# Optimization experiments

Hardware: AMD Instinct MI355X
Metric: run time of the kernel (lower is better)

Reference implementation:

```python
import jax, jax.numpy as jnp
import numpy as np

D_MODEL = 768
NUM_HEADS = 12


def setup_inputs() -> dict:
    key = jax.random.key(0)
    ks = jax.random.split(key, 11)
    B, N, D = 4, 2048, D_MODEL
    s = 1.0 / np.sqrt(D)
    return {
        "q": jax.random.normal(ks[0], (B, N, D), jnp.float32),
        "k": jax.random.normal(ks[1], (B, N, D), jnp.float32),
        "v": jax.random.normal(ks[2], (B, N, D), jnp.float32),
        "wq": jax.random.normal(ks[3], (D, D), jnp.float32) * s,
        "bq": jnp.zeros((D,), jnp.float32),
        "wk": jax.random.normal(ks[4], (D, D), jnp.float32) * s,
        "bk": jnp.zeros((D,), jnp.float32),
        "wv": jax.random.normal(ks[5], (D, D), jnp.float32) * s,
        "bv": jnp.zeros((D,), jnp.float32),
        "wo": jax.random.normal(ks[6], (D, D), jnp.float32) * s,
        "bo": jnp.zeros((D,), jnp.float32),
    }


def _split_heads(x, num_heads):
    B, N, D = x.shape
    hd = D // num_heads
    return x.reshape(B, N, num_heads, hd).transpose(0, 2, 1, 3)  # (B,H,N,hd)


def reference(q, k, v, wq, bq, wk, bk, wv, bv, wo, bo):
    B, N, D = q.shape
    H = NUM_HEADS
    qw = q @ wq.T + bq
    kw = k @ wk.T + bk
    vw = v @ wv.T + bv
    hq = _split_heads(qw, H)
    hk = _split_heads(kw, H)
    hv = _split_heads(vw, H)
    scale = 1.0 / jnp.sqrt(jnp.asarray(hq.shape[-1], hq.dtype))
    scores = jnp.einsum("bhnd,bhmd->bhnm", hq, hk) * scale  # (B,H,N,N) explicit
    attn = jax.nn.softmax(scores, axis=-1)
    out = jnp.einsum("bhnm,bhmd->bhnd", attn, hv)
    out = out.transpose(0, 2, 1, 3).reshape(B, N, D)
    return out @ wo.T + bo
```

## Files before the change

### kernel.cpp

```cpp
#include <hip/hip_runtime.h>
#include <hip/hip_bf16.h>
#include <type_traits>


typedef __attribute__((ext_vector_type(8)))  __bf16 bf16x8;
typedef __attribute__((ext_vector_type(4)))  __bf16 bf16x4;
typedef __attribute__((ext_vector_type(4)))  float  f32x4;
typedef __attribute__((ext_vector_type(16))) float  f32x16;
typedef __attribute__((ext_vector_type(2)))  unsigned u32x2;
typedef __attribute__((ext_vector_type(4)))  unsigned u32x4;

#define NH  12
#define HD  64
#define DM  768
#define SEQ 2048
#define NB  4
#define M8  8192
#define ALPHA 0.18033688011112043f

__device__ __forceinline__ f32x4 mfma16(bf16x8 a, bf16x8 b, f32x4 c) {
  return __builtin_amdgcn_mfma_f32_16x16x32_bf16(a, b, c, 0, 0, 0);
}
__device__ __forceinline__ f32x16 mfma32(bf16x8 a, bf16x8 b, f32x16 c) {
  return __builtin_amdgcn_mfma_f32_32x32x16_bf16(a, b, c, 0, 0, 0);
}
__device__ __forceinline__ void gload16(const void* g, void* l) {
  auto gp = (__attribute__((address_space(1))) void*)(const_cast<void*>(g));
  auto lp = (__attribute__((address_space(3))) void*)(l);
  __builtin_amdgcn_global_load_lds(gp, lp, 16, 0, 0);
}
__device__ __forceinline__ float exp2_(float x) {
#if __has_builtin(__builtin_amdgcn_exp2f)
  return __builtin_amdgcn_exp2f(x);
#else
  return exp2f(x);
#endif
}

#define VMLG(n) do { asm volatile("s_waitcnt vmcnt(" #n ") lgkmcnt(0)" ::: "memory"); \
                     __builtin_amdgcn_sched_barrier(0); } while (0)
#define VMW(n) do { asm volatile("s_waitcnt vmcnt(" #n ")" ::: "memory"); \
                    __builtin_amdgcn_sched_barrier(0); } while (0)
#define BARX do { __builtin_amdgcn_s_barrier(); \
                  __builtin_amdgcn_sched_barrier(0); } while (0)

__device__ __forceinline__ u32x2 pswap(unsigned a, unsigned b) {
#if __has_builtin(__builtin_amdgcn_permlane32_swap)
  return __builtin_amdgcn_permlane32_swap(a, b, false, false);
#else
  u32x2 r;
  unsigned sa = (unsigned)__shfl_xor((int)a, 32), sb = (unsigned)__shfl_xor((int)b, 32);
  int hi = ((int)threadIdx.x >> 5) & 1;
  r[0] = hi ? sb : a;
  r[1] = hi ? b : sa;
  return r;
#endif
}
__device__ __forceinline__ unsigned f2u(float x) { return __builtin_bit_cast(unsigned, x); }
__device__ __forceinline__ float    u2f(unsigned x) { return __builtin_bit_cast(float, x); }
__device__ __forceinline__ float pcomb_sum(float v) {
  u32x2 r = pswap(f2u(v), f2u(v));
  return u2f(r[0]) + u2f(r[1]);
}
__device__ __forceinline__ unsigned pk(float lo, float hi_) {
  unsigned short ua = __builtin_bit_cast(unsigned short, (__bf16)lo);
  unsigned short ub = __builtin_bit_cast(unsigned short, (__bf16)hi_);
  return ((unsigned)ub << 16) | ua;
}

__global__ void cast4_kernel(const float* __restrict__ a, const float* __restrict__ b,
                             const float* __restrict__ c, const float* __restrict__ d,
                             __bf16* __restrict__ oa, __bf16* __restrict__ ob,
                             __bf16* __restrict__ oc, __bf16* __restrict__ od, int n4) {
  int y = blockIdx.y;
  const float* in = y == 0 ? a : y == 1 ? b : y == 2 ? c : d;
  __bf16* out     = y == 0 ? oa : y == 1 ? ob : y == 2 ? oc : od;
  const float sc  = y == 0 ? ALPHA : 1.0f;
  int i = blockIdx.x * 256 + threadIdx.x;
  if (i < n4) {
    float4 v = ((const float4*)in)[i];
    bf16x4 r;
    r[0] = (__bf16)(v.x * sc); r[1] = (__bf16)(v.y * sc);
    r[2] = (__bf16)(v.z * sc); r[3] = (__bf16)(v.w * sc);
    ((bf16x4*)out)[i] = r;
  }
}

__device__ __forceinline__ void proj_body(const float* __restrict__ A,
                                          const __bf16* __restrict__ B,
                                          const float* __restrict__ bias,
                                          __bf16* __restrict__ C,
                                          long m0, long n0, float bscale, bool trans) {
  __shared__ __align__(16) char LDSG[32768];
  const int tid = threadIdx.x;
  const int w = tid >> 6, l = tid & 63;
  const int g = l >> 4, i16 = l & 15;
  const int wr = w >> 1, wc = w & 1;
  const int srow = l >> 2;
  const int kq = l & 3;
  const int swc = kq ^ ((srow >> 1) & 3);

  const __bf16* Bg = B + (n0 + 16 * w + srow) * (long)DM + swc * 8;
  const float*  Ag = A + (m0 + 16 * w + srow) * (long)DM + kq * 8;
  char* const Awr = LDSG + w * 1024 + srow * 64 + swc * 16;

  const int chsw = (g ^ ((i16 >> 1) & 3)) * 16;
  const char* fA = LDSG + (wr * 64 + i16) * 64 + chsw;
  const char* fB = LDSG + 16384 + (wc * 64 + i16) * 64 + chsw;

  f32x4 acc[4][4] = {};
  float4 arA[4], arB[4];
  long kAa = 0, kAb = 32, kB = 0;

  auto LAA = [&]() {
    arA[0] = *(const float4*)(Ag + kAa);
    arA[1] = *(const float4*)(Ag + kAa + 4);
    arA[2] = *(const float4*)(Ag + 64 * (long)DM + kAa);
    arA[3] = *(const float4*)(Ag + 64 * (long)DM + kAa + 4);
    kAa += 64;
  };
  auto LAB = [&]() {
    arB[0] = *(const float4*)(Ag + kAb);
    arB[1] = *(const float4*)(Ag + kAb + 4);
    arB[2] = *(const float4*)(Ag + 64 * (long)DM + kAb);
    arB[3] = *(const float4*)(Ag + 64 * (long)DM + kAb + 4);
    kAb += 64;
  };
  auto SB = [&](int selb) {
    gload16(Bg + kB, LDSG + 16384 + selb + w * 1024);
    gload16(Bg + 64 * (long)DM + kB, LDSG + 16384 + selb + w * 1024 + 4096);
    kB += 32;
  };
  auto WAA = [&](int selb) {
    u32x4 u0, u1;
    u0[0] = pk(arA[0].x, arA[0].y); u0[1] = pk(arA[0].z, arA[0].w);
    u0[2] = pk(arA[1].x, arA[1].y); u0[3] = pk(arA[1].z, arA[1].w);
    u1[0] = pk(arA[2].x, arA[2].y); u1[1] = pk(arA[2].z, arA[2].w);
    u1[2] = pk(arA[3].x, arA[3].y); u1[3] = pk(arA[3].z, arA[3].w);
    *(u32x4*)(Awr + selb) = u0;
    *(u32x4*)(Awr + selb + 4096) = u1;
  };
  auto WAB = [&](int selb) {
    u32x4 u0, u1;
    u0[0] = pk(arB[0].x, arB[0].y); u0[1] = pk(arB[0].z, arB[0].w);
    u0[2] = pk(arB[1].x, arB[1].y); u0[3] = pk(arB[1].z, arB[1].w);
    u1[0] = pk(arB[2].x, arB[2].y); u1[1] = pk(arB[2].z, arB[2].w);
    u1[2] = pk(arB[3].x, arB[3].y); u1[3] = pk(arB[3].z, arB[3].w);
    *(u32x4*)(Awr + selb) = u0;
    *(u32x4*)(Awr + selb + 4096) = u1;
  };

#define PCOMPUTE(SELB) do { \
    bf16x8 af[4], bfr[4]; \
    _Pragma("unroll") for (int m = 0; m < 4; ++m) \
      af[m] = *(const bf16x8*)(fA + (SELB) + m * 1024); \
    _Pragma("unroll") for (int n = 0; n < 4; ++n) \
      bfr[n] = *(const bf16x8*)(fB + (SELB) + n * 1024); \
    __builtin_amdgcn_s_setprio(1); \
    _Pragma("unroll") for (int m = 0; m < 4; ++m) \
      _Pragma("unroll") for (int n = 0; n < 4; ++n) \
        acc[m][n] = mfma16(af[m], bfr[n], acc[m][n]); \
    __builtin_amdgcn_s_setprio(0); } while (0)

  SB(0); LAA(); LAB(); WAA(0);
  asm volatile("s_waitcnt lgkmcnt(0)" ::: "memory");
  __builtin_amdgcn_sched_barrier(0);
  BARX;
#pragma unroll 1
  for (int j = 0; j < 11; ++j) {
    SB(8192); LAA(); PCOMPUTE(0);    WAB(8192); VMLG(4); BARX;
    SB(0);    LAB(); PCOMPUTE(8192); WAA(0);    VMLG(4); BARX;
  }
  SB(8192); PCOMPUTE(0); WAB(8192); VMLG(0); BARX;
  PCOMPUTE(8192);
#undef PCOMPUTE

  if (trans) {
#pragma unroll
    for (int m = 0; m < 4; ++m)
#pragma unroll
      for (int n = 0; n < 4; ++n) {
        const long col = n0 + wc * 64 + n * 16 + i16;
        const float bv = bias[col] * bscale;
        const long row0 = m0 + wr * 64 + m * 16 + g * 4;
        bf16x4 v4;
#pragma unroll
        for (int r = 0; r < 4; ++r) v4[r] = (__bf16)(acc[m][n][r] + bv);
        *(bf16x4*)(C + col * (long)M8 + row0) = v4;
      }
  } else {
#pragma unroll
    for (int m = 0; m < 4; ++m)
#pragma unroll
      for (int n = 0; n < 4; ++n) {
        const long col = n0 + wc * 64 + n * 16 + i16;
        const float bv = bias[col] * bscale;
        const long row0 = m0 + wr * 64 + m * 16 + g * 4;
#pragma unroll
        for (int r = 0; r < 4; ++r)
          C[(row0 + r) * DM + col] = (__bf16)(acc[m][n][r] + bv);
      }
  }
}

__global__ __launch_bounds__(256, 3) void proj3_gemm(
    const float* __restrict__ q, const float* __restrict__ k, const float* __restrict__ v,
    const __bf16* __restrict__ wqb, const __bf16* __restrict__ wkb, const __bf16* __restrict__ wvb,
    const float* __restrict__ bq, const float* __restrict__ bk, const float* __restrict__ bv,
    __bf16* __restrict__ qpj, __bf16* __restrict__ kpj, __bf16* __restrict__ vpT) {
  const int gid = blockIdx.x;
  const int swz = (gid & 7) * 144 + (gid >> 3);
  const int z = swz / 384, rem = swz % 384;
  const long xb = rem / 6, yb = rem % 6;
  const float* A = z == 0 ? q : z == 1 ? k : v;
  const __bf16* B = z == 0 ? wqb : z == 1 ? wkb : wvb;
  const float* bias = z == 0 ? bq : z == 1 ? bk : bv;
  __bf16* C = z == 0 ? qpj : z == 1 ? kpj : vpT;
  proj_body(A, B, bias, C, xb * 128, yb * 128, z == 0 ? ALPHA : 1.0f, z == 2);
}

__global__ __launch_bounds__(256) void out_gemm(const __bf16* __restrict__ A,
                                                const __bf16* __restrict__ B,
                                                const float* __restrict__ bias,
                                                float* __restrict__ C) {
  const int gid = blockIdx.x;
  const int swz = (gid & 7) * 48 + (gid >> 3);
  const long m0 = (swz / 6) * 128, n0 = (swz % 6) * 128;

  __shared__ __align__(16) char LDSG[32768];
  const int tid = threadIdx.x;
  const int w = tid >> 6, l = tid & 63;
  const int g = l >> 4, i16 = l & 15;
  const int wr = w >> 1, wc = w & 1;
  const int srow = l >> 2;
  const int swc = (l & 3) ^ ((srow >> 1) & 3);
  const __bf16* Ag = A + (m0 + 16 * w + srow) * (long)DM + swc * 8;
  const __bf16* Bg = B + (n0 + 16 * w + srow) * (long)DM + swc * 8;
  const int chsw = (g ^ ((i16 >> 1) & 3)) * 16;
  const char* fA = LDSG + (wr * 64 + i16) * 64 + chsw;
  const char* fB = LDSG + 16384 + (wc * 64 + i16) * 64 + chsw;

  f32x4 acc[4][4] = {};
  long kB = 0;

#define GSTAGE(SELB) do { \
    gload16(Ag + kB, LDSG + (SELB) + w * 1024); \
    gload16(Ag + 64 * (long)DM + kB, LDSG + (SELB) + w * 1024 + 4096); \
    gload16(Bg + kB, LDSG + 16384 + (SELB) + w * 1024); \
    gload16(Bg + 64 * (long)DM + kB, LDSG + 16384 + (SELB) + w * 1024 + 4096); \
    kB += 32; } while (0)

#define GCOMPUTE(SELB) do { \
    bf16x8 af[4], bfr[4]; \
    _Pragma("unroll") for (int m = 0; m < 4; ++m) \
      af[m] = *(const bf16x8*)(fA + (SELB) + m * 1024); \
    _Pragma("unroll") for (int n = 0; n < 4; ++n) \
      bfr[n] = *(const bf16x8*)(fB + (SELB) + n * 1024); \
    __builtin_amdgcn_s_setprio(1); \
    _Pragma("unroll") for (int m = 0; m < 4; ++m) \
      _Pragma("unroll") for (int n = 0; n < 4; ++n) \
        acc[m][n] = mfma16(af[m], bfr[n], acc[m][n]); \
    __builtin_amdgcn_s_setprio(0); } while (0)

  GSTAGE(0); GSTAGE(8192);
#pragma unroll 1
  for (int k = 0; k + 128 <= DM; k += 64) {
    VMW(4); BARX; GCOMPUTE(0);    BARX; GSTAGE(0);
    VMW(4); BARX; GCOMPUTE(8192); BARX; GSTAGE(8192);
  }
  VMW(4); BARX; GCOMPUTE(0);
  VMW(0); BARX; GCOMPUTE(8192);
#undef GSTAGE
#undef GCOMPUTE

#pragma unroll
  for (int m = 0; m < 4; ++m)
#pragma unroll
    for (int n = 0; n < 4; ++n) {
      const long col = n0 + wc * 64 + n * 16 + i16;
      const float bv = bias[col];
      const long row0 = m0 + wr * 64 + m * 16 + g * 4;
#pragma unroll
      for (int r = 0; r < 4; ++r)
        C[(row0 + r) * DM + col] = acc[m][n][r] + bv;
    }
}

__global__ __launch_bounds__(128, 2) void attn_fwd(const __bf16* __restrict__ qp,
                                                   const __bf16* __restrict__ kp,
                                                   const __bf16* __restrict__ vpT,
                                                   __bf16* __restrict__ ao) {
  __shared__ __align__(16) __bf16 Ks[2][64 * 64];
  __shared__ __align__(16) __bf16 Vs[2][64 * 64];

  const int wg = blockIdx.x;
  const int xcd = wg & 7;
  const int idx = wg >> 3;
  const int bh = xcd * 6 + (idx >> 4);
  const int qt = idx & 15;
  const int b = bh / NH, h = bh % NH;

  const int tid = threadIdx.x;
  const int w = tid >> 6, l = tid & 63;
  const int l31 = l & 31, hi = l >> 5;

  const long qrow0 = (long)b * SEQ + qt * 128 + w * 64 + l31;
  const __bf16* qb0 = qp + qrow0 * DM + h * HD;
  bf16x8 qf0[4], qf1[4];
#pragma unroll
  for (int kk = 0; kk < 4; ++kk) {
    qf0[kk] = *(const bf16x8*)(qb0 + kk * 16 + hi * 8);
    qf1[kk] = *(const bf16x8*)(qb0 + 32 * DM + kk * 16 + hi * 8);
  }

  f32x16 o00 = {}, o01 = {}, o10 = {}, o11 = {};
  float lsum0 = 0.f, lsum1 = 0.f;

  const int srow = tid >> 3;
  const int schunk = (tid & 7) ^ (srow & 7);
  const __bf16* kbase = kp + ((long)b * SEQ) * DM + h * HD;
  const __bf16* vtb = vpT + (long)(h * HD) * M8 + (long)b * SEQ;

  auto stage = [&](int T, int sel) {
    const long kt = (long)T * 64;
    __bf16* Kd = &Ks[sel][w * 512];
    __bf16* Vd = &Vs[sel][w * 512];
#pragma unroll
    for (int j = 0; j < 4; ++j) {
      gload16(kbase + (kt + 16 * j + srow) * (long)DM + schunk * 8, Kd + j * 1024);
      gload16(vtb + (long)(16 * j + srow) * M8 + kt + schunk * 8, Vd + j * 1024);
    }
  };

  auto compute = [&](const __bf16* Kc, const __bf16* Vc) {
    f32x16 s00 = {}, s01 = {}, s10 = {}, s11 = {};
    __builtin_amdgcn_s_setprio(1);
#pragma unroll
    for (int kk = 0; kk < 4; ++kk) {
      const int sw = ((kk * 2 + hi) ^ (l31 & 7)) * 8;
      bf16x8 kf0 = *(const bf16x8*)&Kc[l31 * 64 + sw];
      s00 = mfma32(kf0, qf0[kk], s00);
      s10 = mfma32(kf0, qf1[kk], s10);
      bf16x8 kf1 = *(const bf16x8*)&Kc[2048 + l31 * 64 + sw];
      s01 = mfma32(kf1, qf0[kk], s01);
      s11 = mfma32(kf1, qf1[kk], s11);
    }
    __builtin_amdgcn_s_setprio(0);

#pragma unroll
    for (int r = 0; r < 16; ++r) s00[r] = exp2_(s00[r]);
#pragma unroll
    for (int r = 0; r < 16; ++r) s01[r] = exp2_(s01[r]);
#pragma unroll
    for (int r = 0; r < 16; ++r) s10[r] = exp2_(s10[r]);
#pragma unroll
    for (int r = 0; r < 16; ++r) s11[r] = exp2_(s11[r]);
    {
      f32x16 ps = s00 + s01;
      const float t0 = (ps[0] + ps[1]) + (ps[2] + ps[3]);
      const float t1 = (ps[4] + ps[5]) + (ps[6] + ps[7]);
      const float t2 = (ps[8] + ps[9]) + (ps[10] + ps[11]);
      const float t3 = (ps[12] + ps[13]) + (ps[14] + ps[15]);
      lsum0 += (t0 + t1) + (t2 + t3);
    }
    {
      f32x16 ps = s10 + s11;
      const float t0 = (ps[0] + ps[1]) + (ps[2] + ps[3]);
      const float t1 = (ps[4] + ps[5]) + (ps[6] + ps[7]);
      const float t2 = (ps[8] + ps[9]) + (ps[10] + ps[11]);
      const float t3 = (ps[12] + ps[13]) + (ps[14] + ps[15]);
      lsum1 += (t0 + t1) + (t2 + t3);
    }

    bf16x8 pf0[4], pf1[4];
#pragma unroll
    for (int ks = 0; ks < 4; ++ks) {
      const int base = 8 * (ks & 1);
      {
        const f32x16& S = (ks < 2) ? s00 : s01;
        unsigned pa = pk(S[base + 0], S[base + 1]);
        unsigned pc = pk(S[base + 2], S[base + 3]);
        unsigned pb = pk(S[base + 4], S[base + 5]);
        unsigned pd = pk(S[base + 6], S[base + 7]);
        u32x2 r02 = pswap(pa, pb);
        u32x2 r13 = pswap(pc, pd);
        u32x4 pw;
        pw[0] = r02[0]; pw[1] = r13[0]; pw[2] = r02[1]; pw[3] = r13[1];
        pf0[ks] = __builtin_bit_cast(bf16x8, pw);
      }
      {
        const f32x16& S = (ks < 2) ? s10 : s11;
        unsigned pa = pk(S[base + 0], S[base + 1]);
        unsigned pc = pk(S[base + 2], S[base + 3]);
        unsigned pb = pk(S[base + 4], S[base + 5]);
        unsigned pd = pk(S[base + 6], S[base + 7]);
        u32x2 r02 = pswap(pa, pb);
        u32x2 r13 = pswap(pc, pd);
        u32x4 pw;
        pw[0] = r02[0]; pw[1] = r13[0]; pw[2] = r02[1]; pw[3] = r13[1];
        pf1[ks] = __builtin_bit_cast(bf16x8, pw);
      }
    }

    __builtin_amdgcn_s_setprio(1);
#pragma unroll
    for (int ks = 0; ks < 4; ++ks) {
      const int sw = ((ks * 2 + hi) ^ (l31 & 7)) * 8;
      bf16x8 vf0 = *(const bf16x8*)&Vc[l31 * 64 + sw];
      o00 = mfma32(vf0, pf0[ks], o00);
      o10 = mfma32(vf0, pf1[ks], o10);
      bf16x8 vf1 = *(const bf16x8*)&Vc[2048 + l31 * 64 + sw];
      o01 = mfma32(vf1, pf0[ks], o01);
      o11 = mfma32(vf1, pf1[ks], o11);
    }
    __builtin_amdgcn_s_setprio(0);
  };

  stage(0, 0);
  __syncthreads();
  for (int t = 0; t < SEQ / 64; t += 2) {
    if (t + 1 < SEQ / 64) stage(t + 1, 1);
    compute(Ks[0], Vs[0]);
    __syncthreads();
    if (t + 2 < SEQ / 64) stage(t + 2, 0);
    compute(Ks[1], Vs[1]);
    __syncthreads();
  }

  const float inv0 = 1.0f / pcomb_sum(lsum0);
  const float inv1 = 1.0f / pcomb_sum(lsum1);
  __bf16* ob0 = ao + qrow0 * DM + h * HD;
  __bf16* ob1 = ob0 + 32 * DM;
#pragma unroll
  for (int rg = 0; rg < 4; ++rg) {
    bf16x4 a0, a1, b0, b1;
#pragma unroll
    for (int j = 0; j < 4; ++j) {
      a0[j] = (__bf16)(o00[rg * 4 + j] * inv0);
      a1[j] = (__bf16)(o01[rg * 4 + j] * inv0);
      b0[j] = (__bf16)(o10[rg * 4 + j] * inv1);
      b1[j] = (__bf16)(o11[rg * 4 + j] * inv1);
    }
    *(bf16x4*)(ob0 + 8 * rg + 4 * hi) = a0;
    *(bf16x4*)(ob0 + 32 + 8 * rg + 4 * hi) = a1;
    *(bf16x4*)(ob1 + 8 * rg + 4 * hi) = b0;
    *(bf16x4*)(ob1 + 32 + 8 * rg + 4 * hi) = b1;
  }
}

extern "C" void kernel_launch(void* const* d_in, const int* in_sizes, int n_in,
                              void* d_out, int out_size, void* d_ws, size_t ws_size,
                              hipStream_t stream) {
  const float* q  = (const float*)d_in[0];
  const float* k  = (const float*)d_in[1];
  const float* v  = (const float*)d_in[2];
  const float* wq = (const float*)d_in[3];
  const float* bq = (const float*)d_in[4];
  const float* wk = (const float*)d_in[5];
  const float* bk = (const float*)d_in[6];
  const float* wv = (const float*)d_in[7];
  const float* bv = (const float*)d_in[8];
  const float* wo = (const float*)d_in[9];
  const float* bo = (const float*)d_in[10];

  const long S = (long)M8 * DM;
  const long W = (long)DM * DM;
  __bf16* ws = (__bf16*)d_ws;
  __bf16 *wqb = ws, *wkb = wqb + W, *wvb = wkb + W, *wob = wvb + W;
  __bf16 *qpj = wob + W, *kpj = qpj + S, *vpT = kpj + S, *aob = vpT + S;

  cast4_kernel<<<dim3((unsigned)(W / 4 / 256), 4), 256, 0, stream>>>(
      wq, wk, wv, wo, wqb, wkb, wvb, wob, (int)(W / 4));

  proj3_gemm<<<1152, 256, 0, stream>>>(q, k, v, wqb, wkb, wvb, bq, bk, bv, qpj, kpj, vpT);

  attn_fwd<<<768, 128, 0, stream>>>(qpj, kpj, vpT, aob);

  out_gemm<<<384, 256, 0, stream>>>(aob, wob, bo, (float*)d_out);
}
```

Before: 152.9 us.

## Load K/V fragments directly from global in attention; halve out-GEMM M tile

The attention kernel no longer stages K and V tiles through double-buffered shared memory with barriers. Each wave instead reads its MFMA operand fragments directly from global memory into registers. This removes LDS traffic and synchronisation, but both waves in a block now fetch the same tiles, and there is no explicit prefetch to overlap load latency. The output projection GEMM switches to 64x128 tiles with twice as many blocks, which improves occupancy and CU coverage at the cost of less reuse of the B operand.

```diff
diff --git a/kernel.cpp b/kernel.cpp
--- a/kernel.cpp
+++ b/kernel.cpp
@@ -224,10 +224,12 @@
                                                 const float* __restrict__ bias,
                                                 float* __restrict__ C) {
   const int gid = blockIdx.x;
-  const int swz = (gid & 7) * 48 + (gid >> 3);
-  const long m0 = (swz / 6) * 128, n0 = (swz % 6) * 128;
-
-  __shared__ __align__(16) char LDSG[32768];
+  const int local = (gid >> 3);
+  const long mt = (gid & 7) * 16 + local / 6;
+  const long nt = local % 6;
+  const long m0 = mt * 64, n0 = nt * 128;
+
+  __shared__ __align__(16) char LDSG[24576];
   const int tid = threadIdx.x;
   const int w = tid >> 6, l = tid & 63;
   const int g = l >> 4, i16 = l & 15;
@@ -237,49 +239,48 @@
   const __bf16* Ag = A + (m0 + 16 * w + srow) * (long)DM + swc * 8;
   const __bf16* Bg = B + (n0 + 16 * w + srow) * (long)DM + swc * 8;
   const int chsw = (g ^ ((i16 >> 1) & 3)) * 16;
-  const char* fA = LDSG + (wr * 64 + i16) * 64 + chsw;
-  const char* fB = LDSG + 16384 + (wc * 64 + i16) * 64 + chsw;
-
-  f32x4 acc[4][4] = {};
+  const char* fA = LDSG + (wr * 32 + i16) * 64 + chsw;
+  const char* fB = LDSG + 8192 + (wc * 64 + i16) * 64 + chsw;
+
+  f32x4 acc[2][4] = {};
   long kB = 0;
 
-#define GSTAGE(SELB) do { \
-    gload16(Ag + kB, LDSG + (SELB) + w * 1024); \
-    gload16(Ag + 64 * (long)DM + kB, LDSG + (SELB) + w * 1024 + 4096); \
-    gload16(Bg + kB, LDSG + 16384 + (SELB) + w * 1024); \
-    gload16(Bg + 64 * (long)DM + kB, LDSG + 16384 + (SELB) + w * 1024 + 4096); \
+#define GSTAGE(S) do { \
+    gload16(Ag + kB, LDSG + (S) * 4096 + w * 1024); \
+    gload16(Bg + kB, LDSG + 8192 + (S) * 8192 + w * 1024); \
+    gload16(Bg + 64 * (long)DM + kB, LDSG + 8192 + (S) * 8192 + w * 1024 + 4096); \
     kB += 32; } while (0)
 
-#define GCOMPUTE(SELB) do { \
-    bf16x8 af[4], bfr[4]; \
-    _Pragma("unroll") for (int m = 0; m < 4; ++m) \
-      af[m] = *(const bf16x8*)(fA + (SELB) + m * 1024); \
+#define GCOMPUTE(S) do { \
+    bf16x8 af[2], bfr[4]; \
+    _Pragma("unroll") for (int m = 0; m < 2; ++m) \
+      af[m] = *(const bf16x8*)(fA + (S) * 4096 + m * 1024); \
     _Pragma("unroll") for (int n = 0; n < 4; ++n) \
-      bfr[n] = *(const bf16x8*)(fB + (SELB) + n * 1024); \
+      bfr[n] = *(const bf16x8*)(fB + (S) * 8192 + n * 1024); \
     __builtin_amdgcn_s_setprio(1); \
-    _Pragma("unroll") for (int m = 0; m < 4; ++m) \
+    _Pragma("unroll") for (int m = 0; m < 2; ++m) \
       _Pragma("unroll") for (int n = 0; n < 4; ++n) \
         acc[m][n] = mfma16(af[m], bfr[n], acc[m][n]); \
     __builtin_amdgcn_s_setprio(0); } while (0)
 
-  GSTAGE(0); GSTAGE(8192);
+  GSTAGE(0); GSTAGE(1);
 #pragma unroll 1
   for (int k = 0; k + 128 <= DM; k += 64) {
-    VMW(4); BARX; GCOMPUTE(0);    BARX; GSTAGE(0);
-    VMW(4); BARX; GCOMPUTE(8192); BARX; GSTAGE(8192);
-  }
-  VMW(4); BARX; GCOMPUTE(0);
-  VMW(0); BARX; GCOMPUTE(8192);
+    VMW(3); BARX; GCOMPUTE(0); BARX; GSTAGE(0);
+    VMW(3); BARX; GCOMPUTE(1); BARX; GSTAGE(1);
+  }
+  VMW(3); BARX; GCOMPUTE(0);
+  VMW(0); BARX; GCOMPUTE(1);
 #undef GSTAGE
 #undef GCOMPUTE
 
 #pragma unroll
-  for (int m = 0; m < 4; ++m)
+  for (int m = 0; m < 2; ++m)
 #pragma unroll
     for (int n = 0; n < 4; ++n) {
       const long col = n0 + wc * 64 + n * 16 + i16;
       const float bv = bias[col];
-      const long row0 = m0 + wr * 64 + m * 16 + g * 4;
+      const long row0 = m0 + wr * 32 + m * 16 + g * 4;
 #pragma unroll
       for (int r = 0; r < 4; ++r)
         C[(row0 + r) * DM + col] = acc[m][n][r] + bv;
@@ -290,9 +291,6 @@
                                                    const __bf16* __restrict__ kp,
                                                    const __bf16* __restrict__ vpT,
                                                    __bf16* __restrict__ ao) {
-  __shared__ __align__(16) __bf16 Ks[2][64 * 64];
-  __shared__ __align__(16) __bf16 Vs[2][64 * 64];
-
   const int wg = blockIdx.x;
   const int xcd = wg & 7;
   const int idx = wg >> 3;
@@ -316,36 +314,36 @@
   f32x16 o00 = {}, o01 = {}, o10 = {}, o11 = {};
   float lsum0 = 0.f, lsum1 = 0.f;
 
-  const int srow = tid >> 3;
-  const int schunk = (tid & 7) ^ (srow & 7);
-  const __bf16* kbase = kp + ((long)b * SEQ) * DM + h * HD;
-  const __bf16* vtb = vpT + (long)(h * HD) * M8 + (long)b * SEQ;
-
-  auto stage = [&](int T, int sel) {
-    const long kt = (long)T * 64;
-    __bf16* Kd = &Ks[sel][w * 512];
-    __bf16* Vd = &Vs[sel][w * 512];
-#pragma unroll
-    for (int j = 0; j < 4; ++j) {
-      gload16(kbase + (kt + 16 * j + srow) * (long)DM + schunk * 8, Kd + j * 1024);
-      gload16(vtb + (long)(16 * j + srow) * M8 + kt + schunk * 8, Vd + j * 1024);
-    }
-  };
-
-  auto compute = [&](const __bf16* Kc, const __bf16* Vc) {
+  const __bf16* kL = kp + ((long)b * SEQ + l31) * DM + h * HD + hi * 8;
+  const __bf16* vL = vpT + ((long)(h * HD) + l31) * M8 + (long)b * SEQ + hi * 8;
+
+  for (int t = 0; t < SEQ / 64; ++t) {
+    const __bf16* kT = kL + (long)t * 64 * DM;
+    const __bf16* vT = vL + t * 64;
+
+    bf16x8 kf[8];
+#pragma unroll
+    for (int kk = 0; kk < 4; ++kk) {
+      kf[kk]     = *(const bf16x8*)(kT + kk * 16);
+      kf[4 + kk] = *(const bf16x8*)(kT + 32 * (long)DM + kk * 16);
+    }
     f32x16 s00 = {}, s01 = {}, s10 = {}, s11 = {};
     __builtin_amdgcn_s_setprio(1);
 #pragma unroll
     for (int kk = 0; kk < 4; ++kk) {
-      const int sw = ((kk * 2 + hi) ^ (l31 & 7)) * 8;
-      bf16x8 kf0 = *(const bf16x8*)&Kc[l31 * 64 + sw];
-      s00 = mfma32(kf0, qf0[kk], s00);
-      s10 = mfma32(kf0, qf1[kk], s10);
-      bf16x8 kf1 = *(const bf16x8*)&Kc[2048 + l31 * 64 + sw];
-      s01 = mfma32(kf1, qf0[kk], s01);
-      s11 = mfma32(kf1, qf1[kk], s11);
+      s00 = mfma32(kf[kk], qf0[kk], s00);
+      s10 = mfma32(kf[kk], qf1[kk], s10);
+      s01 = mfma32(kf[4 + kk], qf0[kk], s01);
+      s11 = mfma32(kf[4 + kk], qf1[kk], s11);
     }
     __builtin_amdgcn_s_setprio(0);
+
+    bf16x8 vf[8];
+#pragma unroll
+    for (int ks = 0; ks < 4; ++ks) {
+      vf[ks]     = *(const bf16x8*)(vT + ks * 16);
+      vf[4 + ks] = *(const bf16x8*)(vT + 32 * (long)M8 + ks * 16);
+    }
 
 #pragma unroll
     for (int r = 0; r < 16; ++r) s00[r] = exp2_(s00[r]);
@@ -405,26 +403,12 @@
     __builtin_amdgcn_s_setprio(1);
 #pragma unroll
     for (int ks = 0; ks < 4; ++ks) {
-      const int sw = ((ks * 2 + hi) ^ (l31 & 7)) * 8;
-      bf16x8 vf0 = *(const bf16x8*)&Vc[l31 * 64 + sw];
-      o00 = mfma32(vf0, pf0[ks], o00);
-      o10 = mfma32(vf0, pf1[ks], o10);
-      bf16x8 vf1 = *(const bf16x8*)&Vc[2048 + l31 * 64 + sw];
-      o01 = mfma32(vf1, pf0[ks], o01);
-      o11 = mfma32(vf1, pf1[ks], o11);
+      o00 = mfma32(vf[ks], pf0[ks], o00);
+      o10 = mfma32(vf[ks], pf1[ks], o10);
+      o01 = mfma32(vf[4 + ks], pf0[ks], o01);
+      o11 = mfma32(vf[4 + ks], pf1[ks], o11);
     }
     __builtin_amdgcn_s_setprio(0);
-  };
-
-  stage(0, 0);
-  __syncthreads();
-  for (int t = 0; t < SEQ / 64; t += 2) {
-    if (t + 1 < SEQ / 64) stage(t + 1, 1);
-    compute(Ks[0], Vs[0]);
-    __syncthreads();
-    if (t + 2 < SEQ / 64) stage(t + 2, 0);
-    compute(Ks[1], Vs[1]);
-    __syncthreads();
   }
 
   const float inv0 = 1.0f / pcomb_sum(lsum0);
@@ -476,5 +460,5 @@
 
   attn_fwd<<<768, 128, 0, stream>>>(qpj, kpj, vpT, aob);
 
-  out_gemm<<<384, 256, 0, stream>>>(aob, wob, bo, (float*)d_out);
-}
+  out_gemm<<<768, 256, 0, stream>>>(aob, wob, bo, (float*)d_out);
+}
```

New measurement: 173.3 us. +13.3%, slower.
